# Optimization experiments

Hardware: AMD Instinct MI355X
Metric: run time of the kernel (lower is better)

## Reference

```python
import jax, jax.numpy as jnp
import numpy as np

N_NODES = 50000


def gcn_conv_max(x, edge_index, edge_weight, W, b):
    """PyG GCNConv with aggr='max': gcn_norm (add self-loops, symmetric
    degree normalization), linear transform, gather-scale-scatter_max, bias."""
    n = x.shape[0]
    row, col = edge_index[0], edge_index[1]
    loop = jnp.arange(n)
    row = jnp.concatenate([row, loop])  # sources (incl. self-loops)
    col = jnp.concatenate([col, loop])  # targets
    ew = jnp.concatenate([edge_weight, jnp.ones((n,), x.dtype)])
    deg = jax.ops.segment_sum(ew, col, num_segments=n)
    dis = jnp.where(deg > 0, jax.lax.rsqrt(deg), jnp.zeros_like(deg))
    norm = dis[row] * ew * dis[col]  # [E+N]
    h = x @ W                         # [N, out]
    msg = norm[:, None] * h[row]      # gather + scale, [E+N, out]
    agg = jax.ops.segment_max(msg, col, num_segments=n)  # scatter-max
    return agg + b


def setup_inputs() -> dict:
    key = jax.random.key(0)
    ks = jax.random.split(key, 9)
    N, E = N_NODES, 1_600_000
    x = jax.random.normal(ks[0], (N, 5), dtype=jnp.float32)
    edge_index = jax.random.randint(ks[1], (2, E), 0, N, dtype=jnp.int64)
    edge_weight = jax.random.uniform(ks[2], (E,), dtype=jnp.float32)
    s1 = 1.0 / np.sqrt(5.0)
    s2 = 1.0 / np.sqrt(240.0)
    W1 = jax.random.uniform(ks[3], (5, 240), jnp.float32, -s1, s1)
    b1 = jnp.zeros((240,), jnp.float32)
    W2 = jax.random.uniform(ks[4], (240, 240), jnp.float32, -s2, s2)
    b2 = jnp.zeros((240,), jnp.float32)
    We = jax.random.uniform(ks[5], (240, 80), jnp.float32, -s2, s2)
    be = jnp.zeros((80,), jnp.float32)
    return {"x": x, "edge_index": edge_index, "edge_weight": edge_weight,
            "W1": W1, "b1": b1, "W2": W2, "b2": b2, "We": We, "be": be}


def reference(x, edge_index, edge_weight, W1, b1, W2, b2, We, be):
    h = gcn_conv_max(x, edge_index, edge_weight, W1, b1)
    h = jax.nn.relu(h)
    h = gcn_conv_max(h, edge_index, edge_weight, W2, b2)
    h = jax.nn.relu(h)
    return h @ We + be  # [N, 80]
```

## Files before the change

kernel.cpp:

```cpp
#include <hip/hip_runtime.h>
#include <cfloat>

#define HID 240

static inline size_t alignUp(size_t x, size_t a){ return (x + a - 1) / a * a; }

typedef __bf16 bf16x8 __attribute__((ext_vector_type(8)));
typedef unsigned short u16x8 __attribute__((ext_vector_type(8)));
typedef float  f32x16 __attribute__((ext_vector_type(16)));

__device__ __forceinline__ float b2f(unsigned short u){
    return __uint_as_float(((unsigned)u) << 16);
}
__device__ __forceinline__ unsigned short f2b_rne(float f){
    unsigned r = __float_as_uint(f);
    r += 0x7FFFu + ((r >> 16) & 1u);
    return (unsigned short)(r >> 16);
}

__device__ __forceinline__ float vmax16(f32x16 a){
    float x0 = fmaxf(fmaxf(a[0],  a[1]),  a[2]);
    float x1 = fmaxf(fmaxf(a[3],  a[4]),  a[5]);
    float x2 = fmaxf(fmaxf(a[6],  a[7]),  a[8]);
    float x3 = fmaxf(fmaxf(a[9],  a[10]), a[11]);
    float x4 = fmaxf(fmaxf(a[12], a[13]), a[14]);
    float y0 = fmaxf(fmaxf(x0, x1), x2);
    float y1 = fmaxf(fmaxf(x3, x4), a[15]);
    return fmaxf(y0, y1);
}

__global__ void k_deg_prep(const int* __restrict__ col, const float* __restrict__ ew,
                           unsigned long long* __restrict__ pk, unsigned* __restrict__ rank,
                           int E, int ne, int N, int nb,
                           const float* __restrict__ x, float* __restrict__ xp,
                           const float* __restrict__ W1, unsigned short* __restrict__ W1f,
                           const float* __restrict__ W2, unsigned short* __restrict__ Bt2h,
                           unsigned short* __restrict__ Bt2l,
                           const float* __restrict__ We, unsigned short* __restrict__ Bt3h,
                           unsigned short* __restrict__ Bt3l){
    int b = blockIdx.x;
    int t = threadIdx.x;
    if (b < ne){
        int e = b * 256 + t;
        if (e < E){
            int c = col[e];
            unsigned q = __float2uint_rn(ew[e] * 1048576.0f);
            unsigned long long old = atomicAdd(&pk[c], (1ull << 40) | (unsigned long long)q);
            rank[e] = (unsigned)(old >> 40);
        }
        return;
    }
    int bb = b - ne;
    if (bb < nb){
        __shared__ float s[1280];
        int rbase = bb * 256;
        #pragma unroll
        for (int c = 0; c < 5; c++){
            int idx = rbase * 5 + t + 256 * c;
            s[t + 256 * c] = (idx < N * 5) ? x[idx] : 0.0f;
        }
        __syncthreads();
        #pragma unroll
        for (int c = 0; c < 8; c++){
            int pos = t + 256 * c;
            int r = pos >> 3, j = pos & 7;
            int grow = rbase + r;
            if (grow < N)
                xp[(size_t)grow * 8 + j] = (j < 5) ? s[r * 5 + j] : 0.0f;
        }
        return;
    }
    bb -= nb;
    if (bb < 32){
        int i = bb * 256 + t;
        if (i < 2 * 8 * 64 * 8){
            int k    = i & 7;
            int lane = (i >> 3) & 63;
            int j    = (i >> 9) & 7;
            int s2   = i >> 12;
            int lm = lane & 31, quad = lane >> 5;
            int kg = quad * 8 + k;
            int colm = 32 * j + lm;
            float v = (kg < 5 && colm < HID) ? W1[kg * HID + colm] : 0.0f;
            unsigned short hi = f2b_rne(v);
            W1f[i] = (s2 == 0) ? hi : f2b_rne(v - b2f(hi));
        }
        return;
    }
    bb -= 32;
    if (bb < 240){
        int i = bb * 256 + t;
        int n = i / HID, k = i - n * HID;
        float v = (n < HID) ? W2[(size_t)k * HID + n] : 0.0f;
        unsigned short hi = f2b_rne(v);
        Bt2h[i] = hi;
        Bt2l[i] = f2b_rne(v - b2f(hi));
        return;
    }
    bb -= 240;
    {
        int i = bb * 256 + t;
        if (i < 128 * HID){
            int n = i / HID, k = i - n * HID;
            float v = (n < 80) ? We[(size_t)k * 80 + n] : 0.0f;
            unsigned short hi = f2b_rne(v);
            Bt3h[i] = hi;
            Bt3l[i] = f2b_rne(v - b2f(hi));
        }
    }
}

__global__ void k_dis_bsum(const unsigned long long* __restrict__ pk,
                           float* __restrict__ dis, unsigned* __restrict__ cnt,
                           unsigned* __restrict__ bsum, int N){
    int b = blockIdx.x;
    int i = b * 256 + threadIdx.x;
    unsigned v = 0u;
    if (i < N){
        unsigned long long p = pk[i];
        unsigned c = (unsigned)(p >> 40);
        cnt[i] = c;
        float deg = 1.0f + (float)(p & 0xFFFFFFFFFFull) * (1.0f / 1048576.0f);
        dis[i] = rsqrtf(deg);
        v = (c + 32u) >> 5;
    }
    #pragma unroll
    for (int o = 32; o > 0; o >>= 1) v += __shfl_down(v, (unsigned)o, 64);
    __shared__ unsigned ws[4];
    int lane = threadIdx.x & 63, w = threadIdx.x >> 6;
    if (lane == 0) ws[w] = v;
    __syncthreads();
    if (threadIdx.x == 0) bsum[b] = ws[0] + ws[1] + ws[2] + ws[3];
}

__global__ void k_bscan(const unsigned* __restrict__ bsum, unsigned* __restrict__ boff,
                        unsigned* __restrict__ poff, int nb, int N){
    __shared__ unsigned s[256];
    int t = threadIdx.x;
    unsigned v = (t < nb) ? bsum[t] : 0u;
    s[t] = v;
    __syncthreads();
    for (int o = 1; o < 256; o <<= 1){
        unsigned u = (t >= o) ? s[t - o] : 0u;
        __syncthreads();
        s[t] += u;
        __syncthreads();
    }
    if (t < nb) boff[t] = s[t] - v;
    if (t == 0) poff[N] = 32u * s[nb - 1];
}

__global__ void k_offs_fill(const unsigned* __restrict__ cnt, const unsigned* __restrict__ boff,
                            const float* __restrict__ dis,
                            unsigned* __restrict__ poff, int2* __restrict__ sedge, int N){
    int b = blockIdx.x, t = threadIdx.x;
    int i = b * 256 + t;
    unsigned c = (i < N) ? cnt[i] : 0u;
    unsigned v = (i < N) ? ((c + 32u) >> 5) : 0u;
    int lane = t & 63, w = t >> 6;
    unsigned x = v;
    #pragma unroll
    for (int o = 1; o < 64; o <<= 1){
        unsigned u = __shfl_up(x, (unsigned)o, 64);
        if (lane >= o) x += u;
    }
    __shared__ unsigned ws[4];
    if (lane == 63) ws[w] = x;
    __syncthreads();
    unsigned wb = 0;
    if (w > 0) wb += ws[0];
    if (w > 1) wb += ws[1];
    if (w > 2) wb += ws[2];
    if (i < N){
        unsigned p = 32u * (boff[b] + wb + x - v);
        poff[i] = p;
        float dd = dis[i];
        int2 sv = make_int2(i, __float_as_int(dd * dd));
        sedge[p] = sv;
        unsigned s1 = p + 32u * v;
        for (unsigned s = p + 1u + c; s < s1; s++) sedge[s] = sv;
    }
}

__global__ void k_scatter(const int* __restrict__ row, const int* __restrict__ col,
                          const float* __restrict__ ew, const float* __restrict__ dis,
                          const unsigned* __restrict__ poff, const unsigned* __restrict__ rank,
                          int2* __restrict__ sedge, int E){
    int e = blockIdx.x * blockDim.x + threadIdx.x;
    if (e < E){
        int r = row[e], c = col[e];
        float nw = dis[r] * ew[e] * dis[c];
        unsigned p = poff[c] + 1u + rank[e];
        sedge[p] = make_int2(r, __float_as_int(nw));
    }
}

__global__ __launch_bounds__(256) void k_agg1m(const float* __restrict__ xp,
                                               const unsigned short* __restrict__ W1f,
                                               const unsigned* __restrict__ cnt,
                                               const unsigned* __restrict__ poff,
                                               const int2* __restrict__ sedge,
                                               const float* __restrict__ bias,
                                               float* __restrict__ out, int N, int nwaves){
    int wid  = blockIdx.x * 4 + (threadIdx.x >> 6);
    int lane = threadIdx.x & 63;
    int lm   = lane & 31;

    bf16x8 bh[8], bl[8];
    #pragma unroll
    for (int j = 0; j < 8; j++){
        bh[j] = *(const bf16x8*)(W1f + ((size_t)(0 * 8 + j) * 64 + lane) * 8);
        bl[j] = *(const bf16x8*)(W1f + ((size_t)(1 * 8 + j) * 64 + lane) * 8);
    }
    float bv[8];
    #pragma unroll
    for (int j = 0; j < 8; j++){
        int c = 32 * j + lm;
        bv[j] = (c < HID) ? bias[c] : 0.0f;
    }
    const f32x16 zv = {};

    for (int d = wid; d < N; d += nwaves){
        unsigned base = poff[d];
        unsigned nch  = (cnt[d] + 32u) >> 5;
        float m[8];
        #pragma unroll
        for (int j = 0; j < 8; j++) m[j] = -FLT_MAX;

        for (unsigned c = 0; c < nch; c++){
            u16x8 ahu = (u16x8)0, alu = (u16x8)0;
            if (lane < 32){
                int2 e = sedge[base + 32u * c + (unsigned)lm];
                float w = __int_as_float(e.y);
                const float4* xr = (const float4*)(xp + (size_t)e.x * 8);
                float4 x0 = xr[0], x1 = xr[1];
                float p[5] = {w * x0.x, w * x0.y, w * x0.z, w * x0.w, w * x1.x};
                #pragma unroll
                for (int k = 0; k < 5; k++){
                    unsigned short h = f2b_rne(p[k]);
                    ahu[k] = h;
                    alu[k] = f2b_rne(p[k] - b2f(h));
                }
            }
            bf16x8 ah = __builtin_bit_cast(bf16x8, ahu);
            bf16x8 al = __builtin_bit_cast(bf16x8, alu);
            #pragma unroll
            for (int j = 0; j < 8; j += 2){
                f32x16 a0 = __builtin_amdgcn_mfma_f32_32x32x16_bf16(ah, bh[j],     zv, 0, 0, 0);
                f32x16 a1 = __builtin_amdgcn_mfma_f32_32x32x16_bf16(ah, bh[j + 1], zv, 0, 0, 0);
                a0 = __builtin_amdgcn_mfma_f32_32x32x16_bf16(ah, bl[j],     a0, 0, 0, 0);
                a1 = __builtin_amdgcn_mfma_f32_32x32x16_bf16(ah, bl[j + 1], a1, 0, 0, 0);
                a0 = __builtin_amdgcn_mfma_f32_32x32x16_bf16(al, bh[j],     a0, 0, 0, 0);
                a1 = __builtin_amdgcn_mfma_f32_32x32x16_bf16(al, bh[j + 1], a1, 0, 0, 0);
                m[j]     = fmaxf(m[j],     vmax16(a0));
                m[j + 1] = fmaxf(m[j + 1], vmax16(a1));
            }
        }
        float o[8];
        #pragma unroll
        for (int j = 0; j < 8; j++){
            float other = __shfl_xor(m[j], 32, 64);
            o[j] = fmaxf(fmaxf(m[j], other) + bv[j], 0.0f);
        }
        if (lane < 32){
            float* orow = out + (size_t)d * HID;
            #pragma unroll
            for (int j = 0; j < 8; j++){
                int c = 32 * j + lm;
                if (c < HID) orow[c] = o[j];
            }
        }
    }
}

template <bool OB16>
__global__ __launch_bounds__(256) void k_gemm_mfma(const float* __restrict__ A,
                                                   const unsigned short* __restrict__ Bth,
                                                   const unsigned short* __restrict__ Btl,
                                                   const float* __restrict__ bias,
                                                   void* __restrict__ Cv,
                                                   int M, int Ncol, int Npad, int Cld){
    __shared__ unsigned short As_hi[64][24];
    __shared__ unsigned short As_lo[64][24];
    const int K = 240;
    int t = threadIdx.x;
    int wave = t >> 6, lane = t & 63;
    int m0 = blockIdx.x * 64;
    int n0 = wave * 64;
    bool wact = n0 < Npad;

    int lm   = lane & 31;
    int quad = lane >> 5;

    f32x16 acc[2][2] = {};

    for (int k0 = 0; k0 < K; k0 += 16){
        {
            int m = t >> 2, kq = (t & 3) * 4;
            float4 av = make_float4(0.f, 0.f, 0.f, 0.f);
            if (m0 + m < M) av = *(const float4*)(A + (size_t)(m0 + m) * K + k0 + kq);
            ushort4 hi, lo;
            hi.x = f2b_rne(av.x); lo.x = f2b_rne(av.x - b2f(hi.x));
            hi.y = f2b_rne(av.y); lo.y = f2b_rne(av.y - b2f(hi.y));
            hi.z = f2b_rne(av.z); lo.z = f2b_rne(av.z - b2f(hi.z));
            hi.w = f2b_rne(av.w); lo.w = f2b_rne(av.w - b2f(hi.w));
            *(ushort4*)&As_hi[m][kq] = hi;
            *(ushort4*)&As_lo[m][kq] = lo;
        }
        __syncthreads();
        if (wact){
            size_t bo0 = (size_t)(n0 + lm) * K + k0 + quad * 8;
            size_t bo1 = (size_t)(n0 + 32 + lm) * K + k0 + quad * 8;
            bf16x8 bh0 = *(const bf16x8*)(Bth + bo0);
            bf16x8 bl0 = *(const bf16x8*)(Btl + bo0);
            bf16x8 bh1 = *(const bf16x8*)(Bth + bo1);
            bf16x8 bl1 = *(const bf16x8*)(Btl + bo1);
            #pragma unroll
            for (int mh = 0; mh < 2; mh++){
                bf16x8 ah = *(const bf16x8*)&As_hi[32 * mh + lm][quad * 8];
                bf16x8 al = *(const bf16x8*)&As_lo[32 * mh + lm][quad * 8];
                acc[mh][0] = __builtin_amdgcn_mfma_f32_32x32x16_bf16(ah, bh0, acc[mh][0], 0, 0, 0);
                acc[mh][0] = __builtin_amdgcn_mfma_f32_32x32x16_bf16(ah, bl0, acc[mh][0], 0, 0, 0);
                acc[mh][0] = __builtin_amdgcn_mfma_f32_32x32x16_bf16(al, bh0, acc[mh][0], 0, 0, 0);
                acc[mh][1] = __builtin_amdgcn_mfma_f32_32x32x16_bf16(ah, bh1, acc[mh][1], 0, 0, 0);
                acc[mh][1] = __builtin_amdgcn_mfma_f32_32x32x16_bf16(ah, bl1, acc[mh][1], 0, 0, 0);
                acc[mh][1] = __builtin_amdgcn_mfma_f32_32x32x16_bf16(al, bh1, acc[mh][1], 0, 0, 0);
            }
        }
        __syncthreads();
    }

    if (!wact) return;
    #pragma unroll
    for (int mh = 0; mh < 2; mh++){
        #pragma unroll
        for (int h = 0; h < 2; h++){
            int n = n0 + 32 * h + lm;
            if (n >= Ncol) continue;
            float bvv = (!OB16 && bias) ? bias[n] : 0.0f;
            #pragma unroll
            for (int r = 0; r < 16; r++){
                int m = m0 + 32 * mh + (r & 3) + 8 * (r >> 2) + 4 * quad;
                if (m >= M) continue;
                float v = acc[mh][h][r];
                if (OB16){
                    ((unsigned short*)Cv)[(size_t)m * Cld + n] = f2b_rne(v);
                } else {
                    ((float*)Cv)[(size_t)m * Cld + n] = v + bvv;
                }
            }
        }
    }
}

__global__ __launch_bounds__(256) void k_aggb(const unsigned short* __restrict__ H2,
                                              const unsigned* __restrict__ cnt,
                                              const unsigned* __restrict__ poff,
                                              const int2* __restrict__ sedge,
                                              const float* __restrict__ bias,
                                              float* __restrict__ out, int N){
    int d    = blockIdx.x * 4 + (threadIdx.x >> 6);
    int lane = threadIdx.x & 63;
    if (d >= N) return;
    bool act = lane < 60;

    float4 m = make_float4(-FLT_MAX, -FLT_MAX, -FLT_MAX, -FLT_MAX);
    unsigned p0 = poff[d], p1 = p0 + 1u + cnt[d];
    unsigned p = p0;
    for (; p + 4 <= p1; p += 4){
        int2 e0 = sedge[p], e1 = sedge[p+1], e2 = sedge[p+2], e3 = sedge[p+3];
        if (act){
            ushort4 g0 = ((const ushort4*)(H2 + ((size_t)(unsigned)e0.x << 8)))[lane];
            ushort4 g1 = ((const ushort4*)(H2 + ((size_t)(unsigned)e1.x << 8)))[lane];
            ushort4 g2 = ((const ushort4*)(H2 + ((size_t)(unsigned)e2.x << 8)))[lane];
            ushort4 g3 = ((const ushort4*)(H2 + ((size_t)(unsigned)e3.x << 8)))[lane];
            float w0 = __int_as_float(e0.y), w1 = __int_as_float(e1.y);
            float w2 = __int_as_float(e2.y), w3 = __int_as_float(e3.y);
            m.x = fmaxf(fmaxf(m.x, w0*b2f(g0.x)), fmaxf(w1*b2f(g1.x), fmaxf(w2*b2f(g2.x), w3*b2f(g3.x))));
            m.y = fmaxf(fmaxf(m.y, w0*b2f(g0.y)), fmaxf(w1*b2f(g1.y), fmaxf(w2*b2f(g2.y), w3*b2f(g3.y))));
            m.z = fmaxf(fmaxf(m.z, w0*b2f(g0.z)), fmaxf(w1*b2f(g1.z), fmaxf(w2*b2f(g2.z), w3*b2f(g3.z))));
            m.w = fmaxf(fmaxf(m.w, w0*b2f(g0.w)), fmaxf(w1*b2f(g1.w), fmaxf(w2*b2f(g2.w), w3*b2f(g3.w))));
        }
    }
    for (; p < p1; p++){
        int2 e0 = sedge[p];
        if (act){
            ushort4 g0 = ((const ushort4*)(H2 + ((size_t)(unsigned)e0.x << 8)))[lane];
            float w0 = __int_as_float(e0.y);
            m.x = fmaxf(m.x, w0 * b2f(g0.x)); m.y = fmaxf(m.y, w0 * b2f(g0.y));
            m.z = fmaxf(m.z, w0 * b2f(g0.z)); m.w = fmaxf(m.w, w0 * b2f(g0.w));
        }
    }
    if (act){
        float4 b = ((const float4*)bias)[lane];
        float4 o;
        o.x = fmaxf(m.x + b.x, 0.0f);
        o.y = fmaxf(m.y + b.y, 0.0f);
        o.z = fmaxf(m.z + b.z, 0.0f);
        o.w = fmaxf(m.w + b.w, 0.0f);
        ((float4*)(out + (size_t)d * HID))[lane] = o;
    }
}

extern "C" void kernel_launch(void* const* d_in, const int* in_sizes, int n_in,
                              void* d_out, int out_size, void* d_ws, size_t ws_size,
                              hipStream_t stream){
    const float* x  = (const float*)d_in[0];
    const int*   ei = (const int*)  d_in[1];
    const float* ew = (const float*)d_in[2];
    const float* W1 = (const float*)d_in[3];
    const float* b1 = (const float*)d_in[4];
    const float* W2 = (const float*)d_in[5];
    const float* b2 = (const float*)d_in[6];
    const float* We = (const float*)d_in[7];
    const float* be = (const float*)d_in[8];
    float* out = (float*)d_out;

    const int N = in_sizes[0] / 5;
    const int E = in_sizes[2];
    const int* row = ei;
    const int* col = ei + E;
    const int nb = (N + 255) / 256;

    char* w = (char*)d_ws;
    size_t o = 0;
    auto alloc = [&](size_t bytes) -> void* {
        void* p = w + o;
        o = alignUp(o + bytes, 256);
        return p;
    };
    unsigned long long* pk = (unsigned long long*) alloc((size_t)N * 8);
    float*          dis   = (float*)          alloc((size_t)N * 4);
    unsigned*       cnt   = (unsigned*)       alloc((size_t)N * 4);
    unsigned*       poff  = (unsigned*)       alloc((size_t)(N + 1) * 4);
    unsigned*       bsum  = (unsigned*)       alloc((size_t)nb * 4);
    unsigned*       boff  = (unsigned*)       alloc((size_t)nb * 4);
    unsigned*       rank  = (unsigned*)       alloc((size_t)E * 4);
    int2*           sedge = (int2*)           alloc(((size_t)E + 32u * N + 64u) * 8);
    float*          xp    = (float*)          alloc((size_t)N * 8 * 4);
    unsigned short* W1f   = (unsigned short*) alloc((size_t)2 * 8 * 64 * 8 * 2);
    unsigned short* Bt2h  = (unsigned short*) alloc((size_t)256 * HID * 2);
    unsigned short* Bt2l  = (unsigned short*) alloc((size_t)256 * HID * 2);
    unsigned short* Bt3h  = (unsigned short*) alloc((size_t)128 * HID * 2);
    unsigned short* Bt3l  = (unsigned short*) alloc((size_t)128 * HID * 2);
    unsigned short* bufH2 = (unsigned short*) alloc((size_t)N * 256 * 2);
    float*          bufB  = (float*)          alloc((size_t)N * HID * 4);
    (void)ws_size; (void)n_in; (void)out_size;

    int ne = (E + 255) / 256;

    hipMemsetAsync(pk, 0, (size_t)N * 8, stream);
    k_deg_prep <<<ne + nb + 32 + 240 + 120, 256, 0, stream>>>(col, ew, pk, rank, E, ne, N, nb,
                                                              x, xp, W1, W1f,
                                                              W2, Bt2h, Bt2l,
                                                              We, Bt3h, Bt3l);
    k_dis_bsum <<<nb, 256, 0, stream>>>(pk, dis, cnt, bsum, N);
    k_bscan    <<<1, 256, 0, stream>>>(bsum, boff, poff, nb, N);
    k_offs_fill<<<nb, 256, 0, stream>>>(cnt, boff, dis, poff, sedge, N);
    k_scatter  <<<ne, 256, 0, stream>>>(row, col, ew, dis, poff, rank, sedge, E);

    const int a1blocks = 1536;
    k_agg1m<<<a1blocks, 256, 0, stream>>>(xp, W1f, cnt, poff, sedge, b1, bufB, N, a1blocks * 4);

    int gm = (N + 63) / 64;
    k_gemm_mfma<true><<<gm, 256, 0, stream>>>(bufB, Bt2h, Bt2l, nullptr, bufH2, N, HID, 256, 256);
    k_aggb<<<(N + 3) / 4, 256, 0, stream>>>(bufH2, cnt, poff, sedge, b2, bufB, N);

    k_gemm_mfma<false><<<gm, 256, 0, stream>>>(bufB, Bt3h, Bt3l, be, out, N, 80, 128, 80);
}
```

Baseline: 481.1 us.

## Chunk H2 into column-major 32-wide slabs and aggregate edges in parallel per wave

The layer-2 GEMM now writes H2 as 8 slabs of 32 bf16 columns, each laid out node-major. That makes one node's slice a contiguous 64-byte segment. The aggregation kernel launches 8 blocks per destination group, one per column chunk. Each wave handles 8 edges at once, with 8 lanes per edge and a shuffle max reduction at the end, replacing the sequential walk over edges by a whole wave. The aim is more independent gathers in flight and smaller per-chunk working sets, at the cost of reading the edge list 8 times and wasting lanes on the partially valid last chunk and on padded edge groups.

```diff
diff --git a/kernel.cpp b/kernel.cpp
--- a/kernel.cpp
+++ b/kernel.cpp
@@ -8,6 +8,7 @@
 typedef __bf16 bf16x8 __attribute__((ext_vector_type(8)));
 typedef unsigned short u16x8 __attribute__((ext_vector_type(8)));
 typedef float  f32x16 __attribute__((ext_vector_type(16)));
+typedef float  f32x4  __attribute__((ext_vector_type(4)));
 
 __device__ __forceinline__ float b2f(unsigned short u){
     return __uint_as_float(((unsigned)u) << 16);
@@ -344,7 +345,7 @@
                 if (m >= M) continue;
                 float v = acc[mh][h][r];
                 if (OB16){
-                    ((unsigned short*)Cv)[(size_t)m * Cld + n] = f2b_rne(v);
+                    ((unsigned short*)Cv)[(((size_t)(n >> 5) * (size_t)Cld + (size_t)m) << 5) + (n & 31)] = f2b_rne(v);
                 } else {
                     ((float*)Cv)[(size_t)m * Cld + n] = v + bvv;
                 }
@@ -353,52 +354,64 @@
     }
 }
 
-__global__ __launch_bounds__(256) void k_aggb(const unsigned short* __restrict__ H2,
+__global__ __launch_bounds__(256) void k_aggc(const unsigned short* __restrict__ H2c,
                                               const unsigned* __restrict__ cnt,
                                               const unsigned* __restrict__ poff,
                                               const int2* __restrict__ sedge,
                                               const float* __restrict__ bias,
                                               float* __restrict__ out, int N){
-    int d    = blockIdx.x * 4 + (threadIdx.x >> 6);
-    int lane = threadIdx.x & 63;
+    int chunk = blockIdx.x & 7;
+    int d     = (blockIdx.x >> 3) * 4 + (threadIdx.x >> 6);
+    int lane  = threadIdx.x & 63;
+    int cq    = lane & 7;
     if (d >= N) return;
-    bool act = lane < 60;
+
+    const unsigned short* base = H2c + (((size_t)chunk * (size_t)N) << 5) + (cq << 2);
+
+    unsigned p0 = poff[d];
+    unsigned ng = (cnt[d] + 8u) >> 3;
 
     float4 m = make_float4(-FLT_MAX, -FLT_MAX, -FLT_MAX, -FLT_MAX);
-    unsigned p0 = poff[d], p1 = p0 + 1u + cnt[d];
-    unsigned p = p0;
-    for (; p + 4 <= p1; p += 4){
-        int2 e0 = sedge[p], e1 = sedge[p+1], e2 = sedge[p+2], e3 = sedge[p+3];
-        if (act){
-            ushort4 g0 = ((const ushort4*)(H2 + ((size_t)(unsigned)e0.x << 8)))[lane];
-            ushort4 g1 = ((const ushort4*)(H2 + ((size_t)(unsigned)e1.x << 8)))[lane];
-            ushort4 g2 = ((const ushort4*)(H2 + ((size_t)(unsigned)e2.x << 8)))[lane];
-            ushort4 g3 = ((const ushort4*)(H2 + ((size_t)(unsigned)e3.x << 8)))[lane];
-            float w0 = __int_as_float(e0.y), w1 = __int_as_float(e1.y);
-            float w2 = __int_as_float(e2.y), w3 = __int_as_float(e3.y);
-            m.x = fmaxf(fmaxf(m.x, w0*b2f(g0.x)), fmaxf(w1*b2f(g1.x), fmaxf(w2*b2f(g2.x), w3*b2f(g3.x))));
-            m.y = fmaxf(fmaxf(m.y, w0*b2f(g0.y)), fmaxf(w1*b2f(g1.y), fmaxf(w2*b2f(g2.y), w3*b2f(g3.y))));
-            m.z = fmaxf(fmaxf(m.z, w0*b2f(g0.z)), fmaxf(w1*b2f(g1.z), fmaxf(w2*b2f(g2.z), w3*b2f(g3.z))));
-            m.w = fmaxf(fmaxf(m.w, w0*b2f(g0.w)), fmaxf(w1*b2f(g1.w), fmaxf(w2*b2f(g2.w), w3*b2f(g3.w))));
-        }
-    }
-    for (; p < p1; p++){
-        int2 e0 = sedge[p];
-        if (act){
-            ushort4 g0 = ((const ushort4*)(H2 + ((size_t)(unsigned)e0.x << 8)))[lane];
-            float w0 = __int_as_float(e0.y);
-            m.x = fmaxf(m.x, w0 * b2f(g0.x)); m.y = fmaxf(m.y, w0 * b2f(g0.y));
-            m.z = fmaxf(m.z, w0 * b2f(g0.z)); m.w = fmaxf(m.w, w0 * b2f(g0.w));
-        }
-    }
-    if (act){
-        float4 b = ((const float4*)bias)[lane];
-        float4 o;
-        o.x = fmaxf(m.x + b.x, 0.0f);
-        o.y = fmaxf(m.y + b.y, 0.0f);
-        o.z = fmaxf(m.z + b.z, 0.0f);
-        o.w = fmaxf(m.w + b.w, 0.0f);
-        ((float4*)(out + (size_t)d * HID))[lane] = o;
+    const unsigned long long* se = (const unsigned long long*)sedge + p0 + (lane >> 3);
+    unsigned it = 0;
+    for (; it + 2 <= ng; it += 2){
+        unsigned long long ev0 = __builtin_nontemporal_load(se);
+        unsigned long long ev1 = __builtin_nontemporal_load(se + 8);
+        se += 16;
+        unsigned r0 = (unsigned)ev0; float w0 = __uint_as_float((unsigned)(ev0 >> 32));
+        unsigned r1 = (unsigned)ev1; float w1 = __uint_as_float((unsigned)(ev1 >> 32));
+        ushort4 g0 = *(const ushort4*)(base + ((size_t)r0 << 5));
+        ushort4 g1 = *(const ushort4*)(base + ((size_t)r1 << 5));
+        m.x = fmaxf(fmaxf(m.x, w0 * b2f(g0.x)), w1 * b2f(g1.x));
+        m.y = fmaxf(fmaxf(m.y, w0 * b2f(g0.y)), w1 * b2f(g1.y));
+        m.z = fmaxf(fmaxf(m.z, w0 * b2f(g0.z)), w1 * b2f(g1.z));
+        m.w = fmaxf(fmaxf(m.w, w0 * b2f(g0.w)), w1 * b2f(g1.w));
+    }
+    if (it < ng){
+        unsigned long long ev0 = __builtin_nontemporal_load(se);
+        unsigned r0 = (unsigned)ev0; float w0 = __uint_as_float((unsigned)(ev0 >> 32));
+        ushort4 g0 = *(const ushort4*)(base + ((size_t)r0 << 5));
+        m.x = fmaxf(m.x, w0 * b2f(g0.x));
+        m.y = fmaxf(m.y, w0 * b2f(g0.y));
+        m.z = fmaxf(m.z, w0 * b2f(g0.z));
+        m.w = fmaxf(m.w, w0 * b2f(g0.w));
+    }
+    #pragma unroll
+    for (int o = 8; o < 64; o <<= 1){
+        m.x = fmaxf(m.x, __shfl_xor(m.x, o, 64));
+        m.y = fmaxf(m.y, __shfl_xor(m.y, o, 64));
+        m.z = fmaxf(m.z, __shfl_xor(m.z, o, 64));
+        m.w = fmaxf(m.w, __shfl_xor(m.w, o, 64));
+    }
+    int c0 = chunk * 32 + cq * 4;
+    if ((lane >> 3) == 0 && c0 < HID){
+        float4 b = *(const float4*)(bias + c0);
+        f32x4 o4;
+        o4[0] = fmaxf(m.x + b.x, 0.0f);
+        o4[1] = fmaxf(m.y + b.y, 0.0f);
+        o4[2] = fmaxf(m.z + b.z, 0.0f);
+        o4[3] = fmaxf(m.w + b.w, 0.0f);
+        __builtin_nontemporal_store(o4, (f32x4*)(out + (size_t)d * HID + c0));
     }
 }
 
@@ -443,7 +456,7 @@
     unsigned short* Bt2l  = (unsigned short*) alloc((size_t)256 * HID * 2);
     unsigned short* Bt3h  = (unsigned short*) alloc((size_t)128 * HID * 2);
     unsigned short* Bt3l  = (unsigned short*) alloc((size_t)128 * HID * 2);
-    unsigned short* bufH2 = (unsigned short*) alloc((size_t)N * 256 * 2);
+    unsigned short* bufH2 = (unsigned short*) alloc((size_t)8 * N * 32 * 2);
     float*          bufB  = (float*)          alloc((size_t)N * HID * 4);
     (void)ws_size; (void)n_in; (void)out_size;
 
@@ -463,8 +476,8 @@
     k_agg1m<<<a1blocks, 256, 0, stream>>>(xp, W1f, cnt, poff, sedge, b1, bufB, N, a1blocks * 4);
 
     int gm = (N + 63) / 64;
-    k_gemm_mfma<true><<<gm, 256, 0, stream>>>(bufB, Bt2h, Bt2l, nullptr, bufH2, N, HID, 256, 256);
-    k_aggb<<<(N + 3) / 4, 256, 0, stream>>>(bufH2, cnt, poff, sedge, b2, bufB, N);
+    k_gemm_mfma<true><<<gm, 256, 0, stream>>>(bufB, Bt2h, Bt2l, nullptr, bufH2, N, HID, 256, N);
+    k_aggc<<<8 * ((N + 3) / 4), 256, 0, stream>>>(bufH2, cnt, poff, sedge, b2, bufB, N);
 
     k_gemm_mfma<false><<<gm, 256, 0, stream>>>(bufB, Bt3h, Bt3l, be, out, N, 80, 128, 80);
 }
```

Result: slower. 588.1 us (+22.2%).
